# Kernel tuning notes

Hardware: AMD Instinct MI355X
Metric: run time of the kernel (lower is better)

## Reference

```python
import jax, jax.numpy as jnp
import numpy as np
from jax import lax

B, C, KH, SH, K = 128, 256, 7, 31, 3
EPS = 1e-5
DN = ('NCHW', 'OIHW', 'NCHW')


def _bn(x, p):
    # p: (4, C) rows = gamma, beta, running_mean, running_var (eval-mode BN)
    g, b, m, v = p[0], p[1], p[2], p[3]
    inv = g / jnp.sqrt(v + EPS)
    return x * inv[None, :, None, None] + (b - m * inv)[None, :, None, None]


def _dwconv(x, w):
    # depthwise 3x3 VALID conv, w: (C,1,K,K)
    return lax.conv_general_dilated(x, w, (1, 1), 'VALID', dimension_numbers=DN,
                                    feature_group_count=x.shape[1])


def _pwconv(x, w, b):
    y = lax.conv_general_dilated(x, w, (1, 1), 'VALID', dimension_numbers=DN)
    return y + b[None, :, None, None]


def _relu6(x):
    return jnp.minimum(jax.nn.relu(x), 6.0)


def _branch(x, dw_w, bn1, pw_w, pw_b, bn2):
    # Conv(dw,3x3,no bias) -> BN -> ReLU6 -> Conv(1x1) -> BN
    return _bn(_pwconv(_relu6(_bn(_dwconv(x, dw_w), bn1)), pw_w, pw_b), bn2)


def _xcorr_depthwise(search, kernel):
    # per-sample, per-channel cross-correlation via groups = B*C conv trick
    b, c, hs, ws = search.shape
    hk, wk = kernel.shape[2], kernel.shape[3]
    x = search.reshape(1, b * c, hs, ws)
    k = kernel.reshape(b * c, 1, hk, wk)
    out = lax.conv_general_dilated(x, k, (1, 1), 'VALID', dimension_numbers=DN,
                                   feature_group_count=b * c)
    return out.reshape(b, c, out.shape[2], out.shape[3])


def _bn_params(key):
    k1, k2, k3, k4 = jax.random.split(key, 4)
    g = jax.random.uniform(k1, (C,), minval=0.5, maxval=1.5)
    b = jax.random.normal(k2, (C,)) * 0.1
    m = jax.random.normal(k3, (C,)) * 0.1
    v = jax.random.uniform(k4, (C,), minval=0.5, maxval=1.5)
    return jnp.stack([g, b, m, v]).astype(jnp.float32)


def setup_inputs() -> dict:
    key = jax.random.key(0)
    ks = jax.random.split(key, 10)
    dw_std = np.float32(np.sqrt(2.0 / (K * K * C)))   # torch init: normal(0, sqrt(2/n))
    pw_std = np.float32(np.sqrt(2.0 / C))
    return {
        'kernel': jax.random.normal(ks[0], (B, C, KH, KH), jnp.float32),
        'search': jax.random.normal(ks[1], (B, C, SH, SH), jnp.float32),
        'k_dw_w': jax.random.normal(ks[2], (C, 1, K, K), jnp.float32) * dw_std,
        'k_bn1': _bn_params(ks[3]),
        'k_pw_w': jax.random.normal(ks[4], (C, C, 1, 1), jnp.float32) * pw_std,
        'k_pw_b': jnp.zeros((C,), jnp.float32),
        'k_bn2': _bn_params(ks[5]),
        's_dw_w': jax.random.normal(ks[6], (C, 1, K, K), jnp.float32) * dw_std,
        's_bn1': _bn_params(ks[7]),
        's_pw_w': jax.random.normal(ks[8], (C, C, 1, 1), jnp.float32) * pw_std,
        's_pw_b': jnp.zeros((C,), jnp.float32),
        's_bn2': _bn_params(ks[9]),
    }


def reference(kernel, search, k_dw_w, k_bn1, k_pw_w, k_pw_b, k_bn2,
              s_dw_w, s_bn1, s_pw_w, s_pw_b, s_bn2):
    k = _branch(kernel, k_dw_w, k_bn1, k_pw_w, k_pw_b, k_bn2)   # (B,C,5,5)
    s = _branch(search, s_dw_w, s_bn1, s_pw_w, s_pw_b, s_bn2)   # (B,C,29,29)
    return _xcorr_depthwise(s, k)                                # (B,C,25,25)
```

## Files before the change

### kernel.cpp

```cpp
#include <hip/hip_runtime.h>

constexpr int B = 128, C = 256;
constexpr float EPS = 1e-5f;
constexpr int NSG = B * 841;
constexpr int NKG = B * 25;

typedef unsigned short u16;
typedef short short8 __attribute__((ext_vector_type(8)));
typedef u16 u16x8 __attribute__((ext_vector_type(8)));
typedef float f32x4 __attribute__((ext_vector_type(4)));

__device__ __forceinline__ u16 bf16_rne(float x) {
    unsigned u = __builtin_bit_cast(unsigned, x);
    return (u16)((u + 0x7FFFu + ((u >> 16) & 1u)) >> 16);
}
__device__ __forceinline__ float bf16_f(u16 h) {
    return __builtin_bit_cast(float, (unsigned)h << 16);
}

__global__ __launch_bounds__(256)
void wprep3(const float* __restrict__ ws, const float* __restrict__ wk,
            u16* __restrict__ WtS, u16* __restrict__ WtK) {
    int i = blockIdx.x * 256 + threadIdx.x;
    int co = i >> 8, k = i & 255;
    int t = k >> 5, cg = co >> 4;
    int lane = ((k >> 3) & 3) * 16 + (co & 15);
    int e = k & 7;
    size_t o = ((size_t)(t * 16 + cg) * 64 + lane) * 8 + e;
    WtS[o] = bf16_rne(ws[i]);
    WtK[o] = bf16_rne(wk[i]);
}

template<int IN_H>
__global__ __launch_bounds__(256)
void dw_pass11(const float* __restrict__ in, const float* __restrict__ dw_w,
               const float* __restrict__ bn1, u16* __restrict__ X3) {
    constexpr int OUT_H = IN_H - 2, ON = OUT_H * OUT_H, IHW = IN_H * IN_H;
    constexpr int NSP = B * ON;
    const int n = blockIdx.z * 256 + threadIdx.x;
    if (n >= ON) return;
    const int b = blockIdx.x, kc = blockIdx.y;
    const int oh = n / OUT_H, ow = n - oh * OUT_H;
    const float* base = in + (((size_t)b * C + kc * 8) * IN_H + oh) * IN_H + ow;

    u16x8 pv;
    #pragma unroll
    for (int cl = 0; cl < 8; ++cl) {
        const int cig = kc * 8 + cl;
        const float* p = base + (size_t)cl * IHW;
        float x0 = p[0],            x1 = p[1],            x2 = p[2];
        float x3 = p[IN_H],         x4 = p[IN_H + 1],     x5 = p[IN_H + 2];
        float x6 = p[2 * IN_H],     x7 = p[2 * IN_H + 1], x8 = p[2 * IN_H + 2];
        const float* wp = dw_w + cig * 9;
        float res = x0 * wp[0] + x1 * wp[1] + x2 * wp[2]
                  + x3 * wp[3] + x4 * wp[4] + x5 * wp[5]
                  + x6 * wp[6] + x7 * wp[7] + x8 * wp[8];
        const float inv = bn1[cig] * rsqrtf(bn1[3 * C + cig] + EPS);
        const float shv = bn1[C + cig] - bn1[2 * C + cig] * inv;
        float y = res * inv + shv;
        y = fminf(fmaxf(y, 0.f), 6.f);
        pv[cl] = bf16_rne(y);
    }
    *(u16x8*)(X3 + ((size_t)kc * NSP + (size_t)b * ON + n) * 8) = pv;
}

template<int IN_H, int CG>
__global__ __launch_bounds__(256)
void dw_pass7(const float* __restrict__ in, const float* __restrict__ dw_w,
              const float* __restrict__ bn1, u16* __restrict__ X3) {
    constexpr int OUT_H = IN_H - 2, ON = OUT_H * OUT_H, IHW = IN_H * IN_H;
    constexpr int NSTRIP = (OUT_H + 7) / 8;
    constexpr int NFLT = CG * IHW;
    constexpr int NF4 = NFLT / 4;
    constexpr int SUBS = CG / 8;
    constexpr int NSP = B * ON;
    constexpr int PADC = CG + 2;
    constexpr unsigned SM_IN = (NFLT + 16) * 4;
    constexpr unsigned SM_XT = (unsigned)ON * PADC * 2;
    constexpr unsigned SMSZ = SM_IN > SM_XT ? SM_IN : SM_XT;
    __shared__ __align__(16) char SMEM[SMSZ];
    float* S = (float*)SMEM;
    u16* xt = (u16*)SMEM;

    const int tid = threadIdx.x;
    const int b = blockIdx.x, g = blockIdx.y;
    const int ci0 = g * CG;
    const float* src = in + ((size_t)b * C + ci0) * IHW;

    for (int q = tid; q < NF4; q += 256)
        ((float4*)S)[q] = ((const float4*)src)[q];
    __syncthreads();

    const bool active = tid < CG * OUT_H;
    int cl = 0, oh = 0;
    if (active) { cl = tid / OUT_H; oh = tid - cl * OUT_H; }
    u16 outv[NSTRIP][8];
    if (active) {
        const int ci = ci0 + cl;
        float wreg[9];
        #pragma unroll
        for (int q = 0; q < 9; ++q) wreg[q] = dw_w[ci * 9 + q];
        const float inv = bn1[ci] * rsqrtf(bn1[3 * C + ci] + EPS);
        const float shv = bn1[C + ci] - bn1[2 * C + ci] * inv;
        #pragma unroll
        for (int s = 0; s < NSTRIP; ++s) {
            float res[8] = {0.f, 0.f, 0.f, 0.f, 0.f, 0.f, 0.f, 0.f};
            #pragma unroll
            for (int dy = 0; dy < 3; ++dy) {
                const float* r = S + cl * IHW + (oh + dy) * IN_H + s * 8;
                float x[10];
                #pragma unroll
                for (int j = 0; j < 10; ++j) x[j] = r[j];
                #pragma unroll
                for (int o = 0; o < 8; ++o)
                    res[o] = fmaf(x[o], wreg[dy * 3],
                              fmaf(x[o + 1], wreg[dy * 3 + 1],
                               fmaf(x[o + 2], wreg[dy * 3 + 2], res[o])));
            }
            #pragma unroll
            for (int o = 0; o < 8; ++o) {
                float y = res[o] * inv + shv;
                y = fminf(fmaxf(y, 0.f), 6.f);
                outv[s][o] = bf16_rne(y);
            }
        }
    }
    __syncthreads();

    if (active) {
        #pragma unroll
        for (int s = 0; s < NSTRIP; ++s) {
            const int ow0 = s * 8;
            #pragma unroll
            for (int o = 0; o < 8; ++o) {
                if (ow0 + o < OUT_H) {
                    int n = oh * OUT_H + ow0 + o;
                    xt[n * PADC + cl] = outv[s][o];
                }
            }
        }
    }
    __syncthreads();

    for (int q = tid; q < ON * SUBS; q += 256) {
        int sub = q / ON, n = q - sub * ON;
        const unsigned* w = (const unsigned*)xt + n * (PADC / 2) + sub * 4;
        uint4 v = {w[0], w[1], w[2], w[3]};
        u16* dst = X3 + ((size_t)(g * SUBS + sub) * NSP + (size_t)b * ON + n) * 8;
        *(uint4*)dst = v;
    }
}

template<int PQ>
__global__ __launch_bounds__(256)
void gemm7(const u16* __restrict__ X3, const u16* __restrict__ Wt,
           const float* __restrict__ pw_b, const float* __restrict__ bn2,
           u16* __restrict__ out) {
    constexpr int NSP = B * PQ;
    const int lane = threadIdx.x & 63, wave = threadIdx.x >> 6;
    const int lh = lane >> 4, ll = lane & 15;
    const int n0 = blockIdx.x * 64;

    f32x4 acc[4][4] = {};
    short8 bx0[4], aw0[4], bx1[4], aw1[4];

#define LOADX(t, bx)                                                            \
    {                                                                           \
        _Pragma("unroll")                                                       \
        for (int j = 0; j < 4; ++j) {                                           \
            size_t off = ((size_t)((t) * 4 + lh) * NSP + n0 + j * 16 + ll) * 8; \
            bx[j] = *(const short8*)(X3 + off);                                 \
        }                                                                       \
    }
#define LOADW(t, aw)                                                            \
    {                                                                           \
        _Pragma("unroll")                                                       \
        for (int i = 0; i < 4; ++i) {                                           \
            size_t off = ((size_t)((t) * 16 + wave * 4 + i) * 64 + lane) * 8;   \
            aw[i] = *(const short8*)(Wt + off);                                 \
        }                                                                       \
    }
#define MM(aw, bx)                                                              \
    {                                                                           \
        _Pragma("unroll")                                                       \
        for (int i = 0; i < 4; ++i) {                                           \
            _Pragma("unroll")                                                   \
            for (int j = 0; j < 4; ++j)                                         \
                acc[i][j] = __builtin_amdgcn_mfma_f32_16x16x32_bf16(aw[i], bx[j], acc[i][j], 0, 0, 0); \
        }                                                                       \
    }

    LOADX(0, bx0); LOADW(0, aw0);
    #pragma unroll
    for (int tt = 0; tt < 8; tt += 2) {
        if (tt + 1 < 8) { LOADX(tt + 1, bx1); LOADW(tt + 1, aw1); }
        MM(aw0, bx0);
        if (tt + 2 < 8) { LOADX(tt + 2, bx0); LOADW(tt + 2, aw0); }
        if (tt + 1 < 8) { MM(aw1, bx1); }
    }
#undef LOADX
#undef LOADW
#undef MM

    int bj[4], pj[4];
    #pragma unroll
    for (int j = 0; j < 4; ++j) {
        int nn = n0 + j * 16 + ll;
        bj[j] = nn / PQ; pj[j] = nn - bj[j] * PQ;
    }
    #pragma unroll
    for (int i = 0; i < 4; ++i) {
        #pragma unroll
        for (int r = 0; r < 4; ++r) {
            int co = wave * 64 + i * 16 + lh * 4 + r;
            float inv = bn2[co] * rsqrtf(bn2[3 * C + co] + EPS);
            float sh  = bn2[C + co] - bn2[2 * C + co] * inv + pw_b[co] * inv;
            #pragma unroll
            for (int j = 0; j < 4; ++j)
                out[((size_t)bj[j] * C + co) * PQ + pj[j]] = bf16_rne(acc[i][j][r] * inv + sh);
        }
    }
}

__global__ __launch_bounds__(256)
void xcorr3(const u16* __restrict__ s, const u16* __restrict__ k,
            float* __restrict__ out) {
    const int bc0 = blockIdx.x * 10;
    const int nbc = min(10, B * C - bc0);
    __shared__ float ss[10 * 841];
    __shared__ float ks[10 * 25];
    const int tid = threadIdx.x;
    for (int i = tid; i < nbc * 841; i += 256) ss[i] = bf16_f(s[(size_t)bc0 * 841 + i]);
    for (int i = tid; i < nbc * 25; i += 256) ks[i] = bf16_f(k[(size_t)bc0 * 25 + i]);
    __syncthreads();

    const int lb = tid / 25, lt = tid - lb * 25;
    if (lb >= nbc) return;
    const int ohg = lt / 5, owg = lt - ohg * 5;
    const float* sp = ss + lb * 841 + (ohg * 5) * 29 + owg * 5;
    float kk[25];
    #pragma unroll
    for (int q = 0; q < 25; ++q) kk[q] = ks[lb * 25 + q];

    float acc[5][5] = {};
    #pragma unroll
    for (int ir = 0; ir < 9; ++ir) {
        float row[9];
        #pragma unroll
        for (int j = 0; j < 9; ++j) row[j] = sp[ir * 29 + j];
        #pragma unroll
        for (int oi = 0; oi < 5; ++oi) {
            int ki = ir - oi;
            if (ki < 0 || ki > 4) continue;
            #pragma unroll
            for (int oj = 0; oj < 5; ++oj)
                #pragma unroll
                for (int kj = 0; kj < 5; ++kj)
                    acc[oi][oj] = fmaf(row[oj + kj], kk[ki * 5 + kj], acc[oi][oj]);
        }
    }
    float* op = out + (size_t)(bc0 + lb) * 625;
    #pragma unroll
    for (int oi = 0; oi < 5; ++oi)
        #pragma unroll
        for (int oj = 0; oj < 5; ++oj)
            op[(ohg * 5 + oi) * 25 + owg * 5 + oj] = acc[oi][oj];
}

template<int IN_H>
__global__ __launch_bounds__(256)
void branch_fallback(const float* __restrict__ in, const float* __restrict__ dw_w,
                     const float* __restrict__ bn1, const float* __restrict__ pw_w,
                     const float* __restrict__ pw_b, const float* __restrict__ bn2,
                     float* __restrict__ out) {
    constexpr int OUT_H = IN_H - 2;
    constexpr int P = OUT_H * OUT_H;
    const int n0  = blockIdx.x * 64;
    const int co0 = blockIdx.y * 64;
    const int tid = threadIdx.x;
    const int tx = tid & 15, ty = tid >> 4;
    __shared__ __align__(16) float Ws[16][64];
    __shared__ __align__(16) float Xs2[16][64];
    float acc[4][4] = {};
    for (int k0 = 0; k0 < C; k0 += 16) {
        #pragma unroll
        for (int e = 0; e < 4; e++) {
            int idx = e * 256 + tid;
            int m = idx & 63, kk = idx >> 6;
            Ws[kk][m] = pw_w[(co0 + m) * C + (k0 + kk)];
        }
        #pragma unroll
        for (int e = 0; e < 4; e++) {
            int idx = e * 256 + tid;
            int nn = idx & 63, kk = idx >> 6;
            int ci = k0 + kk;
            int n = n0 + nn;
            int b = n / P, p = n - b * P;
            int oh = p / OUT_H, ow = p - oh * OUT_H;
            const float* ip = in + (((size_t)b * C + ci) * IN_H + oh) * IN_H + ow;
            const float* wp = dw_w + ci * 9;
            float s = 0.f;
            #pragma unroll
            for (int dy = 0; dy < 3; dy++)
                #pragma unroll
                for (int dx = 0; dx < 3; dx++)
                    s = fmaf(ip[dy * IN_H + dx], wp[dy * 3 + dx], s);
            float inv = bn1[ci] * rsqrtf(bn1[3 * C + ci] + EPS);
            float y = s * inv + (bn1[C + ci] - bn1[2 * C + ci] * inv);
            Xs2[kk][nn] = fminf(fmaxf(y, 0.f), 6.f);
        }
        __syncthreads();
        #pragma unroll
        for (int kk = 0; kk < 16; kk++) {
            float4 av = *reinterpret_cast<const float4*>(&Ws[kk][ty * 4]);
            float4 bv = *reinterpret_cast<const float4*>(&Xs2[kk][tx * 4]);
            float a[4] = {av.x, av.y, av.z, av.w};
            float bb[4] = {bv.x, bv.y, bv.z, bv.w};
            #pragma unroll
            for (int i = 0; i < 4; i++)
                #pragma unroll
                for (int j = 0; j < 4; j++)
                    acc[i][j] = fmaf(a[i], bb[j], acc[i][j]);
        }
        __syncthreads();
    }
    #pragma unroll
    for (int i = 0; i < 4; i++) {
        int co = co0 + ty * 4 + i;
        float inv = bn2[co] * rsqrtf(bn2[3 * C + co] + EPS);
        float sh  = (bn2[C + co] - bn2[2 * C + co] * inv) + pw_b[co] * inv;
        int n = n0 + tx * 4;
        #pragma unroll
        for (int j = 0; j < 4; j++) {
            int nj = n + j;
            int bj2 = nj / P, pj2 = nj - bj2 * P;
            out[((size_t)bj2 * C + co) * P + pj2] = acc[i][j] * inv + sh;
        }
    }
}

__global__ __launch_bounds__(256)
void xcorr2f(const float* __restrict__ s, const float* __restrict__ k,
             float* __restrict__ out) {
    const int bc0 = blockIdx.x * 10;
    const int nbc = min(10, B * C - bc0);
    __shared__ float ss[10 * 841];
    __shared__ float ks[10 * 25];
    const int tid = threadIdx.x;
    for (int i = tid; i < nbc * 841; i += 256) ss[i] = s[(size_t)bc0 * 841 + i];
    for (int i = tid; i < nbc * 25; i += 256) ks[i] = k[(size_t)bc0 * 25 + i];
    __syncthreads();
    const int lb = tid / 25, lt = tid - lb * 25;
    if (lb >= nbc) return;
    const int ohg = lt / 5, owg = lt - ohg * 5;
    const float* sp = ss + lb * 841 + (ohg * 5) * 29 + owg * 5;
    float kk[25];
    #pragma unroll
    for (int q = 0; q < 25; ++q) kk[q] = ks[lb * 25 + q];
    float acc[5][5] = {};
    #pragma unroll
    for (int ir = 0; ir < 9; ++ir) {
        float row[9];
        #pragma unroll
        for (int j = 0; j < 9; ++j) row[j] = sp[ir * 29 + j];
        #pragma unroll
        for (int oi = 0; oi < 5; ++oi) {
            int ki = ir - oi;
            if (ki < 0 || ki > 4) continue;
            #pragma unroll
            for (int oj = 0; oj < 5; ++oj)
                #pragma unroll
                for (int kj = 0; kj < 5; ++kj)
                    acc[oi][oj] = fmaf(row[oj + kj], kk[ki * 5 + kj], acc[oi][oj]);
        }
    }
    float* op = out + (size_t)(bc0 + lb) * 625;
    #pragma unroll
    for (int oi = 0; oi < 5; ++oi)
        #pragma unroll
        for (int oj = 0; oj < 5; ++oj)
            op[(ohg * 5 + oi) * 25 + owg * 5 + oj] = acc[oi][oj];
}

extern "C" void kernel_launch(void* const* d_in, const int* in_sizes, int n_in,
                              void* d_out, int out_size, void* d_ws, size_t ws_size,
                              hipStream_t stream) {
    const float* kernel = (const float*)d_in[0];
    const float* search = (const float*)d_in[1];
    const float* k_dw_w = (const float*)d_in[2];
    const float* k_bn1  = (const float*)d_in[3];
    const float* k_pw_w = (const float*)d_in[4];
    const float* k_pw_b = (const float*)d_in[5];
    const float* k_bn2  = (const float*)d_in[6];
    const float* s_dw_w = (const float*)d_in[7];
    const float* s_bn1  = (const float*)d_in[8];
    const float* s_pw_w = (const float*)d_in[9];
    const float* s_pw_b = (const float*)d_in[10];
    const float* s_bn2  = (const float*)d_in[11];

    constexpr size_t SB_B  = (size_t)NSG * C * 2;
    constexpr size_t KB_B  = (size_t)NKG * C * 2;
    constexpr size_t X3S_B = (size_t)NSG * C * 2;
    constexpr size_t X3K_B = (size_t)NKG * C * 2;
    constexpr size_t W_B   = (size_t)C * C * 2;
    constexpr size_t NEED  = SB_B + KB_B + X3S_B + X3K_B + 2 * W_B;

    if (ws_size >= NEED) {
        char* base = (char*)d_ws;
        u16* Sb   = (u16*)base;   base += SB_B;
        u16* Kb   = (u16*)base;   base += KB_B;
        u16* X3s  = (u16*)base;   base += X3S_B;
        u16* X3k  = (u16*)base;   base += X3K_B;
        u16* WtS  = (u16*)base;   base += W_B;
        u16* WtK  = (u16*)base;

        wprep3<<<dim3(256), dim3(256), 0, stream>>>(s_pw_w, k_pw_w, WtS, WtK);
        dw_pass11<31><<<dim3(B, 32, 4), dim3(256), 0, stream>>>(search, s_dw_w, s_bn1, X3s);
        dw_pass7<7, 32><<<dim3(B, 8), dim3(256), 0, stream>>>(kernel, k_dw_w, k_bn1, X3k);
        gemm7<841><<<dim3(NSG / 64), dim3(256), 0, stream>>>(X3s, WtS, s_pw_b, s_bn2, Sb);
        gemm7<25><<<dim3(NKG / 64), dim3(256), 0, stream>>>(X3k, WtK, k_pw_b, k_bn2, Kb);
        xcorr3<<<dim3((B * C + 9) / 10), dim3(256), 0, stream>>>(Sb, Kb, (float*)d_out);
    } else {
        float* s_buf = (float*)d_ws;
        float* k_buf = s_buf + (size_t)B * C * 29 * 29;
        branch_fallback<7><<<dim3(50, 4), dim3(256), 0, stream>>>(
            kernel, k_dw_w, k_bn1, k_pw_w, k_pw_b, k_bn2, k_buf);
        branch_fallback<31><<<dim3(1682, 4), dim3(256), 0, stream>>>(
            search, s_dw_w, s_bn1, s_pw_w, s_pw_b, s_bn2, s_buf);
        xcorr2f<<<dim3((B * C + 9) / 10), dim3(256), 0, stream>>>(s_buf, k_buf, (float*)d_out);
    }
}
```

Before: 171.6 us.

## Fuse search-branch depthwise conv into pointwise MFMA GEMM via LDS double buffer

Replaces the separate depthwise pass and pointwise GEMM for the search branch with one kernel. Each block computes depthwise+BN+ReLU6 for a 64-position tile in 32-channel slices straight into double-buffered LDS, then feeds those slices to bf16 MFMAs. This removes the round trip of the bf16 X3 intermediate through global memory and one launch. In exchange, every block recomputes its depthwise inputs with strided fp32 loads (9 per channel, uncoalesced across the batch boundary), and the GEMM now waits on that production inside its loop.

After: 243.4 us. 1.42x slower.

```diff
diff --git a/kernel.cpp b/kernel.cpp
--- a/kernel.cpp
+++ b/kernel.cpp
@@ -31,37 +31,93 @@
     WtK[o] = bf16_rne(wk[i]);
 }
 
-template<int IN_H>
-__global__ __launch_bounds__(256)
-void dw_pass11(const float* __restrict__ in, const float* __restrict__ dw_w,
-               const float* __restrict__ bn1, u16* __restrict__ X3) {
-    constexpr int OUT_H = IN_H - 2, ON = OUT_H * OUT_H, IHW = IN_H * IN_H;
-    constexpr int NSP = B * ON;
-    const int n = blockIdx.z * 256 + threadIdx.x;
-    if (n >= ON) return;
-    const int b = blockIdx.x, kc = blockIdx.y;
-    const int oh = n / OUT_H, ow = n - oh * OUT_H;
-    const float* base = in + (((size_t)b * C + kc * 8) * IN_H + oh) * IN_H + ow;
-
-    u16x8 pv;
-    #pragma unroll
-    for (int cl = 0; cl < 8; ++cl) {
-        const int cig = kc * 8 + cl;
-        const float* p = base + (size_t)cl * IHW;
-        float x0 = p[0],            x1 = p[1],            x2 = p[2];
-        float x3 = p[IN_H],         x4 = p[IN_H + 1],     x5 = p[IN_H + 2];
-        float x6 = p[2 * IN_H],     x7 = p[2 * IN_H + 1], x8 = p[2 * IN_H + 2];
-        const float* wp = dw_w + cig * 9;
-        float res = x0 * wp[0] + x1 * wp[1] + x2 * wp[2]
-                  + x3 * wp[3] + x4 * wp[4] + x5 * wp[5]
-                  + x6 * wp[6] + x7 * wp[7] + x8 * wp[8];
-        const float inv = bn1[cig] * rsqrtf(bn1[3 * C + cig] + EPS);
-        const float shv = bn1[C + cig] - bn1[2 * C + cig] * inv;
-        float y = res * inv + shv;
-        y = fminf(fmaxf(y, 0.f), 6.f);
-        pv[cl] = bf16_rne(y);
-    }
-    *(u16x8*)(X3 + ((size_t)kc * NSP + (size_t)b * ON + n) * 8) = pv;
+__global__ __launch_bounds__(256)
+void fgemm(const float* __restrict__ in, const float* __restrict__ dw_w,
+           const float* __restrict__ bn1, const u16* __restrict__ Wt,
+           const float* __restrict__ pw_b, const float* __restrict__ bn2,
+           u16* __restrict__ out) {
+    constexpr int IN_H = 31, OUT_H = 29, ON = 841, IHW = IN_H * IN_H;
+    constexpr int PQ = ON;
+    const int lane = threadIdx.x & 63, wave = threadIdx.x >> 6;
+    const int lh = lane >> 4, ll = lane & 15;
+    const int n0 = blockIdx.x * 64;
+
+    const int nl = threadIdx.x & 63;
+    const int glb = threadIdx.x >> 6;
+    const int n = n0 + nl;
+    const int pb = n / ON, pp = n - pb * ON;
+    const int oh = pp / OUT_H, ow = pp - oh * OUT_H;
+    const float* ibase = in + (((size_t)pb * C) * IN_H + oh) * IN_H + ow;
+
+    __shared__ __align__(16) u16 XS[2][4 * 64 * 8];
+
+    auto produce = [&](int d, int t) {
+        const int ci0 = t * 32 + glb * 8;
+        u16x8 pv;
+        #pragma unroll
+        for (int cl = 0; cl < 8; ++cl) {
+            const int ci = ci0 + cl;
+            const float* p = ibase + (size_t)ci * IHW;
+            float x0 = p[0],        x1 = p[1],            x2 = p[2];
+            float x3 = p[IN_H],     x4 = p[IN_H + 1],     x5 = p[IN_H + 2];
+            float x6 = p[2 * IN_H], x7 = p[2 * IN_H + 1], x8 = p[2 * IN_H + 2];
+            const float* wp = dw_w + ci * 9;
+            float res = x0 * wp[0] + x1 * wp[1] + x2 * wp[2]
+                      + x3 * wp[3] + x4 * wp[4] + x5 * wp[5]
+                      + x6 * wp[6] + x7 * wp[7] + x8 * wp[8];
+            const float inv = bn1[ci] * rsqrtf(bn1[3 * C + ci] + EPS);
+            const float shv = bn1[C + ci] - bn1[2 * C + ci] * inv;
+            float y = res * inv + shv;
+            y = fminf(fmaxf(y, 0.f), 6.f);
+            pv[cl] = bf16_rne(y);
+        }
+        *(u16x8*)&XS[d][((size_t)glb * 64 + nl) * 8] = pv;
+    };
+
+    f32x4 acc[4][4] = {};
+    produce(0, 0);
+    __syncthreads();
+
+    #pragma unroll 1
+    for (int t = 0; t < 8; ++t) {
+        const int d = t & 1;
+        short8 bx[4];
+        #pragma unroll
+        for (int j = 0; j < 4; ++j)
+            bx[j] = *(const short8*)&XS[d][((size_t)lh * 64 + j * 16 + ll) * 8];
+        short8 aw[4];
+        #pragma unroll
+        for (int i = 0; i < 4; ++i) {
+            size_t off = ((size_t)(t * 16 + wave * 4 + i) * 64 + lane) * 8;
+            aw[i] = *(const short8*)(Wt + off);
+        }
+        if (t + 1 < 8) produce(d ^ 1, t + 1);
+        #pragma unroll
+        for (int i = 0; i < 4; ++i)
+            #pragma unroll
+            for (int j = 0; j < 4; ++j)
+                acc[i][j] = __builtin_amdgcn_mfma_f32_16x16x32_bf16(aw[i], bx[j], acc[i][j], 0, 0, 0);
+        __syncthreads();
+    }
+
+    int bj[4], pj[4];
+    #pragma unroll
+    for (int j = 0; j < 4; ++j) {
+        int nn = n0 + j * 16 + ll;
+        bj[j] = nn / PQ; pj[j] = nn - bj[j] * PQ;
+    }
+    #pragma unroll
+    for (int i = 0; i < 4; ++i) {
+        #pragma unroll
+        for (int r = 0; r < 4; ++r) {
+            int co = wave * 64 + i * 16 + lh * 4 + r;
+            float inv = bn2[co] * rsqrtf(bn2[3 * C + co] + EPS);
+            float sh  = bn2[C + co] - bn2[2 * C + co] * inv + pw_b[co] * inv;
+            #pragma unroll
+            for (int j = 0; j < 4; ++j)
+                out[((size_t)bj[j] * C + co) * PQ + pj[j]] = bf16_rne(acc[i][j][r] * inv + sh);
+        }
+    }
 }
 
 template<int IN_H, int CG>
@@ -400,24 +456,22 @@
 
     constexpr size_t SB_B  = (size_t)NSG * C * 2;
     constexpr size_t KB_B  = (size_t)NKG * C * 2;
-    constexpr size_t X3S_B = (size_t)NSG * C * 2;
     constexpr size_t X3K_B = (size_t)NKG * C * 2;
     constexpr size_t W_B   = (size_t)C * C * 2;
-    constexpr size_t NEED  = SB_B + KB_B + X3S_B + X3K_B + 2 * W_B;
+    constexpr size_t NEED  = SB_B + KB_B + X3K_B + 2 * W_B;
 
     if (ws_size >= NEED) {
         char* base = (char*)d_ws;
         u16* Sb   = (u16*)base;   base += SB_B;
         u16* Kb   = (u16*)base;   base += KB_B;
-        u16* X3s  = (u16*)base;   base += X3S_B;
         u16* X3k  = (u16*)base;   base += X3K_B;
         u16* WtS  = (u16*)base;   base += W_B;
         u16* WtK  = (u16*)base;
 
         wprep3<<<dim3(256), dim3(256), 0, stream>>>(s_pw_w, k_pw_w, WtS, WtK);
-        dw_pass11<31><<<dim3(B, 32, 4), dim3(256), 0, stream>>>(search, s_dw_w, s_bn1, X3s);
+        fgemm<<<dim3(NSG / 64), dim3(256), 0, stream>>>(
+            search, s_dw_w, s_bn1, WtS, s_pw_b, s_bn2, Sb);
         dw_pass7<7, 32><<<dim3(B, 8), dim3(256), 0, stream>>>(kernel, k_dw_w, k_bn1, X3k);
-        gemm7<841><<<dim3(NSG / 64), dim3(256), 0, stream>>>(X3s, WtS, s_pw_b, s_bn2, Sb);
         gemm7<25><<<dim3(NKG / 64), dim3(256), 0, stream>>>(X3k, WtK, k_pw_b, k_bn2, Kb);
         xcorr3<<<dim3((B * C + 9) / 10), dim3(256), 0, stream>>>(Sb, Kb, (float*)d_out);
     } else {
```
